# Kernel tuning notes

Measured on AMD Instinct MI355X. Metric: run time of the kernel, lower is better.

The kernel has to match this reference:

```python
import jax, jax.numpy as jnp
import numpy as np

N, D = 16384, 2048


def setup_inputs() -> dict:
    key = jax.random.key(0)
    k1, k2, k3, k4 = jax.random.split(key, 4)
    X = jax.random.normal(k1, (N, D), dtype=jnp.float32)
    keep = jax.random.uniform(k4, (N, D)) > 0.5
    X = jnp.where(keep, X, 0.0)
    A = jax.random.normal(k2, (D, D), dtype=jnp.float32)
    b = jax.random.normal(k3, (D,), dtype=jnp.float32)
    return {"X": X, "A": A, "b": b}


def reference(X, A, b):
    # y_pred = X @ A.T + b
    y_pred = jnp.einsum('nd,kd->nk', X, A) + b  # [N, D]
    mask = X != 0
    masked = jnp.where(mask, y_pred, 0.0)
    row_sum = masked.sum(axis=1, keepdims=True)          # [N, 1]
    has_any = mask.any(axis=1, keepdims=True)            # [N, 1]
    y_out = jnp.where(mask, masked / row_sum, 0.0)
    # rows with an empty mask stay all-zero (matches the Python-loop guard)
    y_out = jnp.where(has_any, y_out, 0.0)
    return y_out
```

## Files before the change

kernel.cpp:

```cpp
#include <hip/hip_runtime.h>

#define N_ROWS 16384
#define D_DIM  2048
#define BM 128
#define BN 128
#define BK 32
#define NKT (D_DIM / BK)

typedef __attribute__((ext_vector_type(8)))  _Float16 half8;
typedef __attribute__((ext_vector_type(4)))  _Float16 half4_t;
typedef __attribute__((ext_vector_type(4)))  float floatx4;

typedef __attribute__((address_space(1))) const unsigned int as1_uint;
typedef __attribute__((address_space(3))) unsigned int as3_uint;

__device__ __forceinline__ void gload_lds16(const _Float16* g, _Float16* l) {
    __builtin_amdgcn_global_load_lds((as1_uint*)g, (as3_uint*)l, 16, 0, 0);
}

__global__ void split_all_kernel(const float4* __restrict__ Xs,
                                 half4_t* __restrict__ Xdh,
                                 half4_t* __restrict__ Xdl,
                                 unsigned char* __restrict__ mask,
                                 const float4* __restrict__ As,
                                 half4_t* __restrict__ Adh,
                                 half4_t* __restrict__ Adl,
                                 int nX8, int total8)
{
    int i = blockIdx.x * blockDim.x + threadIdx.x;
    if (i >= total8) return;

    const float4* src; half4_t* dh; half4_t* dl; int j; bool domask;
    if (i < nX8) { src = Xs; dh = Xdh; dl = Xdl; j = i;       domask = true;  }
    else         { src = As; dh = Adh; dl = Adl; j = i - nX8; domask = false; }

    float4 a = src[2 * j];
    float4 b = src[2 * j + 1];
    half4_t ha, la, hb, lb;
    ha[0] = (_Float16)a.x; ha[1] = (_Float16)a.y;
    ha[2] = (_Float16)a.z; ha[3] = (_Float16)a.w;
    la[0] = (_Float16)((a.x - (float)ha[0]) * 4096.0f);
    la[1] = (_Float16)((a.y - (float)ha[1]) * 4096.0f);
    la[2] = (_Float16)((a.z - (float)ha[2]) * 4096.0f);
    la[3] = (_Float16)((a.w - (float)ha[3]) * 4096.0f);
    hb[0] = (_Float16)b.x; hb[1] = (_Float16)b.y;
    hb[2] = (_Float16)b.z; hb[3] = (_Float16)b.w;
    lb[0] = (_Float16)((b.x - (float)hb[0]) * 4096.0f);
    lb[1] = (_Float16)((b.y - (float)hb[1]) * 4096.0f);
    lb[2] = (_Float16)((b.z - (float)hb[2]) * 4096.0f);
    lb[3] = (_Float16)((b.w - (float)hb[3]) * 4096.0f);
    dh[2 * j] = ha; dh[2 * j + 1] = hb;
    dl[2 * j] = la; dl[2 * j + 1] = lb;
    if (domask) {
        unsigned int m = 0;
        m |= (a.x != 0.0f) ? 0x01u : 0u;  m |= (a.y != 0.0f) ? 0x02u : 0u;
        m |= (a.z != 0.0f) ? 0x04u : 0u;  m |= (a.w != 0.0f) ? 0x08u : 0u;
        m |= (b.x != 0.0f) ? 0x10u : 0u;  m |= (b.y != 0.0f) ? 0x20u : 0u;
        m |= (b.z != 0.0f) ? 0x40u : 0u;  m |= (b.w != 0.0f) ? 0x80u : 0u;
        mask[j] = (unsigned char)m;
    }
}

__global__ __launch_bounds__(256, 2)
void gemm_presplit_kernel(const _Float16* __restrict__ Xh,
                          const _Float16* __restrict__ Xl,
                          const _Float16* __restrict__ Ah,
                          const _Float16* __restrict__ Al,
                          const unsigned char* __restrict__ maskbits,
                          const float* __restrict__ bias,
                          float* __restrict__ out,
                          float* __restrict__ partials)
{
    __shared__ __align__(16) _Float16 sXh[2][BM * BK];
    __shared__ __align__(16) _Float16 sXl[2][BM * BK];
    __shared__ __align__(16) _Float16 sAh[2][BN * BK];
    __shared__ __align__(16) _Float16 sAl[2][BN * BK];

    const int t   = threadIdx.x;
    const int bid = blockIdx.x;

    const int xcd    = bid & 7;
    const int local  = bid >> 3;
    const int r_tile = (xcd << 4) + (local & 15);
    const int c_tile = local >> 4;
    const int m0 = r_tile * BM;
    const int n0 = c_tile * BN;

    const int lane  = t & 63;
    const int w     = t >> 6;
    const int wr    = w >> 1;
    const int wc    = w & 1;
    const int lrow  = lane & 15;
    const int lslot = lane >> 4;

    floatx4 acc1[4][4], acc2[4][4];
    #pragma unroll
    for (int mi = 0; mi < 4; ++mi)
        #pragma unroll
        for (int ni = 0; ni < 4; ++ni)
            #pragma unroll
            for (int j = 0; j < 4; ++j) { acc1[mi][ni][j] = 0.f; acc2[mi][ni][j] = 0.f; }

    const _Float16* gsrc;
    _Float16* lb0; _Float16* lb1;
    if      (w == 0) { gsrc = Xh + (size_t)m0 * D_DIM; lb0 = &sXh[0][0]; lb1 = &sXh[1][0]; }
    else if (w == 1) { gsrc = Xl + (size_t)m0 * D_DIM; lb0 = &sXl[0][0]; lb1 = &sXl[1][0]; }
    else if (w == 2) { gsrc = Ah + (size_t)n0 * D_DIM; lb0 = &sAh[0][0]; lb1 = &sAh[1][0]; }
    else             { gsrc = Al + (size_t)n0 * D_DIM; lb0 = &sAl[0][0]; lb1 = &sAl[1][0]; }

    int off8[8];
    #pragma unroll
    for (int i = 0; i < 8; ++i) {
        int c = i * 64 + lane;
        int row = c >> 2;
        int sp  = c & 3;
        int kslot = sp ^ ((row >> 1) & 3);
        off8[i] = row * D_DIM + kslot * 8;
    }

    auto issue = [&](int buf, int kt) {
        _Float16* lb = buf ? lb1 : lb0;
        const _Float16* gk = gsrc + kt * BK;
        #pragma unroll
        for (int i = 0; i < 8; ++i)
            gload_lds16(gk + off8[i], lb + i * 512);
    };

    issue(0, 0);

    int cur = 0;
    for (int kt = 0; kt < NKT; ++kt) {
        __syncthreads();
        if (kt + 1 < NKT) issue(cur ^ 1, kt + 1);

        half8 bhf[4], blf[4];
        #pragma unroll
        for (int ni = 0; ni < 4; ++ni) {
            int row = wc * 64 + ni * 16 + lrow;
            int off = row * BK + ((lslot ^ ((row >> 1) & 3)) << 3);
            bhf[ni] = *reinterpret_cast<const half8*>(&sAh[cur][off]);
            blf[ni] = *reinterpret_cast<const half8*>(&sAl[cur][off]);
        }
        #pragma unroll
        for (int mi = 0; mi < 4; ++mi) {
            int row = wr * 64 + mi * 16 + lrow;
            int off = row * BK + ((lslot ^ ((row >> 1) & 3)) << 3);
            half8 ah = *reinterpret_cast<const half8*>(&sXh[cur][off]);
            half8 al = *reinterpret_cast<const half8*>(&sXl[cur][off]);
            #pragma unroll
            for (int ni = 0; ni < 4; ++ni) {
                acc1[mi][ni] = __builtin_amdgcn_mfma_f32_16x16x32_f16(ah, bhf[ni], acc1[mi][ni], 0, 0, 0);
                acc2[mi][ni] = __builtin_amdgcn_mfma_f32_16x16x32_f16(ah, blf[ni], acc2[mi][ni], 0, 0, 0);
                acc2[mi][ni] = __builtin_amdgcn_mfma_f32_16x16x32_f16(al, bhf[ni], acc2[mi][ni], 0, 0, 0);
            }
        }
        cur ^= 1;
    }

    #pragma unroll
    for (int mi = 0; mi < 4; ++mi) {
        float rs[4];
        #pragma unroll
        for (int j = 0; j < 4; ++j) rs[j] = 0.f;
        #pragma unroll
        for (int ni = 0; ni < 4; ++ni) {
            int c = n0 + wc * 64 + ni * 16 + lrow;
            float bv = bias[c];
            #pragma unroll
            for (int j = 0; j < 4; ++j) {
                int r = m0 + wr * 64 + mi * 16 + lslot * 4 + j;
                size_t idx = (size_t)r * D_DIM + c;
                float v = acc1[mi][ni][j] + acc2[mi][ni][j] * (1.0f / 4096.0f) + bv;
                unsigned int bit = (maskbits[idx >> 3] >> (c & 7)) & 1u;
                float mv = bit ? v : 0.0f;
                out[idx] = mv;
                rs[j] += mv;
            }
        }
        #pragma unroll
        for (int j = 0; j < 4; ++j) {
            float s = rs[j];
            s += __shfl_xor(s, 1, 64);
            s += __shfl_xor(s, 2, 64);
            s += __shfl_xor(s, 4, 64);
            s += __shfl_xor(s, 8, 64);
            if (lrow == 0) {
                int r = m0 + wr * 64 + mi * 16 + lslot * 4 + j;
                partials[(size_t)r * 32 + c_tile * 2 + wc] = s;
            }
        }
    }
}

__global__ void scale_fused_kernel(float* __restrict__ out,
                                   const float* __restrict__ partials)
{
    int r   = blockIdx.x * 8 + (threadIdx.x >> 5);
    int l32 = threadIdx.x & 31;
    float s = partials[(size_t)r * 32 + l32];
    s += __shfl_xor(s, 1, 32);
    s += __shfl_xor(s, 2, 32);
    s += __shfl_xor(s, 4, 32);
    s += __shfl_xor(s, 8, 32);
    s += __shfl_xor(s, 16, 32);
    float inv = (s != 0.0f) ? (1.0f / s) : 0.0f;
    float4* rowp = reinterpret_cast<float4*>(out + (size_t)r * D_DIM);
    #pragma unroll
    for (int j = 0; j < 16; ++j) {
        float4 v = rowp[j * 32 + l32];
        v.x *= inv; v.y *= inv; v.z *= inv; v.w *= inv;
        rowp[j * 32 + l32] = v;
    }
}

__global__ __launch_bounds__(256, 2)
void gemm_mask_kernel(const float* __restrict__ X,
                      const float* __restrict__ A,
                      const float* __restrict__ bias,
                      float* __restrict__ out)
{
    __shared__ __align__(16) _Float16 sXh[2][BM * BK];
    __shared__ __align__(16) _Float16 sXl[2][BM * BK];
    __shared__ __align__(16) _Float16 sAh[2][BN * BK];
    __shared__ __align__(16) _Float16 sAl[2][BN * BK];

    const int t   = threadIdx.x;
    const int bid = blockIdx.x;
    const int xcd    = bid & 7;
    const int local  = bid >> 3;
    const int r_tile = (xcd << 4) + (local & 15);
    const int c_tile = local >> 4;
    const int m0 = r_tile * BM;
    const int n0 = c_tile * BN;

    const int lane  = t & 63;
    const int w     = t >> 6;
    const int wr    = w >> 1;
    const int wc    = w & 1;
    const int lrow  = lane & 15;
    const int lslot = lane >> 4;

    const float4* X4 = reinterpret_cast<const float4*>(X);
    const float4* A4 = reinterpret_cast<const float4*>(A);

    floatx4 acc1[4][4], acc2[4][4];
    #pragma unroll
    for (int mi = 0; mi < 4; ++mi)
        #pragma unroll
        for (int ni = 0; ni < 4; ++ni)
            #pragma unroll
            for (int j = 0; j < 4; ++j) { acc1[mi][ni][j] = 0.f; acc2[mi][ni][j] = 0.f; }

    float4 rx[4], ra[4];
    #pragma unroll
    for (int i = 0; i < 4; ++i) {
        int f = i * 256 + t; int row = f >> 3; int k4 = f & 7;
        rx[i] = X4[(size_t)(m0 + row) * (D_DIM / 4) + k4];
        ra[i] = A4[(size_t)(n0 + row) * (D_DIM / 4) + k4];
    }

    auto stage = [&](const float4* rv, _Float16* dsh, _Float16* dsl) {
        #pragma unroll
        for (int i = 0; i < 4; ++i) {
            int f = i * 256 + t; int row = f >> 3; int k4 = f & 7;
            float4 v = rv[i];
            half4_t h, l;
            h[0] = (_Float16)v.x; h[1] = (_Float16)v.y;
            h[2] = (_Float16)v.z; h[3] = (_Float16)v.w;
            l[0] = (_Float16)((v.x - (float)h[0]) * 4096.0f);
            l[1] = (_Float16)((v.y - (float)h[1]) * 4096.0f);
            l[2] = (_Float16)((v.z - (float)h[2]) * 4096.0f);
            l[3] = (_Float16)((v.w - (float)h[3]) * 4096.0f);
            int off = row * BK + ((((k4 >> 1) ^ ((row >> 1) & 3)) << 3) + ((k4 & 1) << 2));
            *reinterpret_cast<half4_t*>(dsh + off) = h;
            *reinterpret_cast<half4_t*>(dsl + off) = l;
        }
    };

    stage(rx, &sXh[0][0], &sXl[0][0]);
    stage(ra, &sAh[0][0], &sAl[0][0]);

    int cur = 0;
    for (int kt = 0; kt < NKT; ++kt) {
        __syncthreads();
        const bool more = (kt + 1 < NKT);
        if (more) {
            int kb = (kt + 1) * (BK / 4);
            #pragma unroll
            for (int i = 0; i < 4; ++i) {
                int f = i * 256 + t; int row = f >> 3; int k4 = f & 7;
                rx[i] = X4[(size_t)(m0 + row) * (D_DIM / 4) + kb + k4];
                ra[i] = A4[(size_t)(n0 + row) * (D_DIM / 4) + kb + k4];
            }
        }

        half8 bhf[4], blf[4];
        #pragma unroll
        for (int ni = 0; ni < 4; ++ni) {
            int row = wc * 64 + ni * 16 + lrow;
            int off = row * BK + ((lslot ^ ((row >> 1) & 3)) << 3);
            bhf[ni] = *reinterpret_cast<const half8*>(&sAh[cur][off]);
            blf[ni] = *reinterpret_cast<const half8*>(&sAl[cur][off]);
        }
        #pragma unroll
        for (int mi = 0; mi < 4; ++mi) {
            int row = wr * 64 + mi * 16 + lrow;
            int off = row * BK + ((lslot ^ ((row >> 1) & 3)) << 3);
            half8 ah = *reinterpret_cast<const half8*>(&sXh[cur][off]);
            half8 al = *reinterpret_cast<const half8*>(&sXl[cur][off]);
            #pragma unroll
            for (int ni = 0; ni < 4; ++ni) {
                acc1[mi][ni] = __builtin_amdgcn_mfma_f32_16x16x32_f16(ah, bhf[ni], acc1[mi][ni], 0, 0, 0);
                acc2[mi][ni] = __builtin_amdgcn_mfma_f32_16x16x32_f16(ah, blf[ni], acc2[mi][ni], 0, 0, 0);
                acc2[mi][ni] = __builtin_amdgcn_mfma_f32_16x16x32_f16(al, bhf[ni], acc2[mi][ni], 0, 0, 0);
            }
        }

        if (more) {
            int nxt = cur ^ 1;
            stage(rx, &sXh[nxt][0], &sXl[nxt][0]);
            stage(ra, &sAh[nxt][0], &sAl[nxt][0]);
            cur = nxt;
        }
    }

    #pragma unroll
    for (int mi = 0; mi < 4; ++mi) {
        #pragma unroll
        for (int ni = 0; ni < 4; ++ni) {
            int c = n0 + wc * 64 + ni * 16 + lrow;
            float bv = bias[c];
            #pragma unroll
            for (int j = 0; j < 4; ++j) {
                int r = m0 + wr * 64 + mi * 16 + lslot * 4 + j;
                float v = acc1[mi][ni][j] + acc2[mi][ni][j] * (1.0f / 4096.0f) + bv;
                float xv = X[(size_t)r * D_DIM + c];
                out[(size_t)r * D_DIM + c] = (xv != 0.0f) ? v : 0.0f;
            }
        }
    }
}

__global__ void row_sum_inv_kernel(const float* __restrict__ out, float* __restrict__ inv)
{
    int gw = (blockIdx.x * 256 + threadIdx.x) >> 6;
    int l  = threadIdx.x & 63;
    const float4* row = reinterpret_cast<const float4*>(out) + (size_t)gw * (D_DIM / 4);
    float s = 0.f;
    #pragma unroll
    for (int j = 0; j < 8; ++j) {
        float4 v = row[j * 64 + l];
        s += (v.x + v.y) + (v.z + v.w);
    }
    #pragma unroll
    for (int off = 32; off > 0; off >>= 1) s += __shfl_down(s, off, 64);
    if (l == 0) inv[gw] = (s != 0.0f) ? (1.0f / s) : 0.0f;
}

__global__ void scale_kernel(float* __restrict__ out, const float* __restrict__ inv)
{
    const int total = N_ROWS * (D_DIM / 4);
    float4* o = reinterpret_cast<float4*>(out);
    for (int i = blockIdx.x * blockDim.x + threadIdx.x; i < total;
         i += gridDim.x * blockDim.x) {
        float s  = inv[i >> 9];
        float4 v = o[i];
        v.x *= s; v.y *= s; v.z *= s; v.w *= s;
        o[i] = v;
    }
}

extern "C" void kernel_launch(void* const* d_in, const int* in_sizes, int n_in,
                              void* d_out, int out_size, void* d_ws, size_t ws_size,
                              hipStream_t stream)
{
    const float* X  = (const float*)d_in[0];
    const float* A  = (const float*)d_in[1];
    const float* b  = (const float*)d_in[2];
    float* out = (float*)d_out;

    const size_t nX = (size_t)N_ROWS * D_DIM;
    const size_t nA = (size_t)D_DIM * D_DIM;
    const size_t part_bytes = (size_t)N_ROWS * 32 * sizeof(float);
    const size_t mask_bytes = nX / 8;
    const size_t need = part_bytes + 2 * nX * 2 + 2 * nA * 2 + mask_bytes;

    if (ws_size >= need) {
        float*         part = (float*)d_ws;
        _Float16*      Xh   = (_Float16*)((char*)d_ws + part_bytes);
        _Float16*      Xl   = Xh + nX;
        _Float16*      Ah   = Xl + nX;
        _Float16*      Al   = Ah + nA;
        unsigned char* mb   = (unsigned char*)(Al + nA);

        const int nX8    = (int)(nX / 8);
        const int total8 = (int)((nX + nA) / 8);
        hipLaunchKernelGGL(split_all_kernel, dim3((total8 + 255) / 256), dim3(256), 0, stream,
                           (const float4*)X, (half4_t*)Xh, (half4_t*)Xl, mb,
                           (const float4*)A, (half4_t*)Ah, (half4_t*)Al,
                           nX8, total8);
        hipLaunchKernelGGL(gemm_presplit_kernel, dim3((N_ROWS / BM) * (D_DIM / BN)), dim3(256), 0, stream,
                           Xh, Xl, Ah, Al, mb, b, out, part);
        hipLaunchKernelGGL(scale_fused_kernel, dim3(N_ROWS / 8), dim3(256), 0, stream,
                           out, part);
    } else {
        float* inv = (float*)d_ws;
        hipLaunchKernelGGL(gemm_mask_kernel, dim3((N_ROWS / BM) * (D_DIM / BN)), dim3(256), 0, stream,
                           X, A, b, out);
        hipLaunchKernelGGL(row_sum_inv_kernel, dim3(N_ROWS / 4), dim3(256), 0, stream, out, inv);
        hipLaunchKernelGGL(scale_kernel, dim3(2048), dim3(256), 0, stream, out, inv);
    }
}
```

Measured before the change: 475.2 us.

## Use 8 waves per GEMM block with 2x4 warp layout

Doubles the GEMM workgroup from 256 to 512 threads. Each wave now covers a 64x32 output sub-tile instead of 64x64, and the async global-to-LDS loads are split across twice as many waves. Per-row partial sums widen from 32 to 64 per row, and the scale kernel is adjusted to reduce 64 partials per row with one wave. The intent is more waves per CU to hide latency and lower accumulator register pressure, at the cost of fewer MFMAs per LDS fragment load (less register-level reuse of the A fragments).

```diff
diff --git a/kernel.cpp b/kernel.cpp
--- a/kernel.cpp
+++ b/kernel.cpp
@@ -61,15 +61,15 @@
     }
 }
 
-__global__ __launch_bounds__(256, 2)
-void gemm_presplit_kernel(const _Float16* __restrict__ Xh,
-                          const _Float16* __restrict__ Xl,
-                          const _Float16* __restrict__ Ah,
-                          const _Float16* __restrict__ Al,
-                          const unsigned char* __restrict__ maskbits,
-                          const float* __restrict__ bias,
-                          float* __restrict__ out,
-                          float* __restrict__ partials)
+__global__ __launch_bounds__(512, 2)
+void gemm_presplit8_kernel(const _Float16* __restrict__ Xh,
+                           const _Float16* __restrict__ Xl,
+                           const _Float16* __restrict__ Ah,
+                           const _Float16* __restrict__ Al,
+                           const unsigned char* __restrict__ maskbits,
+                           const float* __restrict__ bias,
+                           float* __restrict__ out,
+                           float* __restrict__ partials)
 {
     __shared__ __align__(16) _Float16 sXh[2][BM * BK];
     __shared__ __align__(16) _Float16 sXl[2][BM * BK];
@@ -88,42 +88,44 @@
 
     const int lane  = t & 63;
     const int w     = t >> 6;
-    const int wr    = w >> 1;
-    const int wc    = w & 1;
+    const int wr    = w >> 2;
+    const int wc    = w & 3;
     const int lrow  = lane & 15;
     const int lslot = lane >> 4;
 
-    floatx4 acc1[4][4], acc2[4][4];
+    floatx4 acc1[4][2], acc2[4][2];
     #pragma unroll
     for (int mi = 0; mi < 4; ++mi)
         #pragma unroll
-        for (int ni = 0; ni < 4; ++ni)
+        for (int ni = 0; ni < 2; ++ni)
             #pragma unroll
             for (int j = 0; j < 4; ++j) { acc1[mi][ni][j] = 0.f; acc2[mi][ni][j] = 0.f; }
 
     const _Float16* gsrc;
     _Float16* lb0; _Float16* lb1;
-    if      (w == 0) { gsrc = Xh + (size_t)m0 * D_DIM; lb0 = &sXh[0][0]; lb1 = &sXh[1][0]; }
-    else if (w == 1) { gsrc = Xl + (size_t)m0 * D_DIM; lb0 = &sXl[0][0]; lb1 = &sXl[1][0]; }
-    else if (w == 2) { gsrc = Ah + (size_t)n0 * D_DIM; lb0 = &sAh[0][0]; lb1 = &sAh[1][0]; }
-    else             { gsrc = Al + (size_t)n0 * D_DIM; lb0 = &sAl[0][0]; lb1 = &sAl[1][0]; }
-
-    int off8[8];
-    #pragma unroll
-    for (int i = 0; i < 8; ++i) {
-        int c = i * 64 + lane;
+    const int arr = w & 3;
+    if      (arr == 0) { gsrc = Xh + (size_t)m0 * D_DIM; lb0 = &sXh[0][0]; lb1 = &sXh[1][0]; }
+    else if (arr == 1) { gsrc = Xl + (size_t)m0 * D_DIM; lb0 = &sXl[0][0]; lb1 = &sXl[1][0]; }
+    else if (arr == 2) { gsrc = Ah + (size_t)n0 * D_DIM; lb0 = &sAh[0][0]; lb1 = &sAh[1][0]; }
+    else               { gsrc = Al + (size_t)n0 * D_DIM; lb0 = &sAl[0][0]; lb1 = &sAl[1][0]; }
+    const int cbase = (w >> 2) * 256;
+
+    int off4[4];
+    #pragma unroll
+    for (int i = 0; i < 4; ++i) {
+        int c = cbase + i * 64 + lane;
         int row = c >> 2;
         int sp  = c & 3;
         int kslot = sp ^ ((row >> 1) & 3);
-        off8[i] = row * D_DIM + kslot * 8;
+        off4[i] = row * D_DIM + kslot * 8;
     }
 
     auto issue = [&](int buf, int kt) {
-        _Float16* lb = buf ? lb1 : lb0;
+        _Float16* lb = (buf ? lb1 : lb0) + cbase * 8;
         const _Float16* gk = gsrc + kt * BK;
         #pragma unroll
-        for (int i = 0; i < 8; ++i)
-            gload_lds16(gk + off8[i], lb + i * 512);
+        for (int i = 0; i < 4; ++i)
+            gload_lds16(gk + off4[i], lb + i * 512);
     };
 
     issue(0, 0);
@@ -133,10 +135,10 @@
         __syncthreads();
         if (kt + 1 < NKT) issue(cur ^ 1, kt + 1);
 
-        half8 bhf[4], blf[4];
-        #pragma unroll
-        for (int ni = 0; ni < 4; ++ni) {
-            int row = wc * 64 + ni * 16 + lrow;
+        half8 bhf[2], blf[2];
+        #pragma unroll
+        for (int ni = 0; ni < 2; ++ni) {
+            int row = wc * 32 + ni * 16 + lrow;
             int off = row * BK + ((lslot ^ ((row >> 1) & 3)) << 3);
             bhf[ni] = *reinterpret_cast<const half8*>(&sAh[cur][off]);
             blf[ni] = *reinterpret_cast<const half8*>(&sAl[cur][off]);
@@ -148,7 +150,7 @@
             half8 ah = *reinterpret_cast<const half8*>(&sXh[cur][off]);
             half8 al = *reinterpret_cast<const half8*>(&sXl[cur][off]);
             #pragma unroll
-            for (int ni = 0; ni < 4; ++ni) {
+            for (int ni = 0; ni < 2; ++ni) {
                 acc1[mi][ni] = __builtin_amdgcn_mfma_f32_16x16x32_f16(ah, bhf[ni], acc1[mi][ni], 0, 0, 0);
                 acc2[mi][ni] = __builtin_amdgcn_mfma_f32_16x16x32_f16(ah, blf[ni], acc2[mi][ni], 0, 0, 0);
                 acc2[mi][ni] = __builtin_amdgcn_mfma_f32_16x16x32_f16(al, bhf[ni], acc2[mi][ni], 0, 0, 0);
@@ -163,8 +165,8 @@
         #pragma unroll
         for (int j = 0; j < 4; ++j) rs[j] = 0.f;
         #pragma unroll
-        for (int ni = 0; ni < 4; ++ni) {
-            int c = n0 + wc * 64 + ni * 16 + lrow;
+        for (int ni = 0; ni < 2; ++ni) {
+            int c = n0 + wc * 32 + ni * 16 + lrow;
             float bv = bias[c];
             #pragma unroll
             for (int j = 0; j < 4; ++j) {
@@ -186,7 +188,7 @@
             s += __shfl_xor(s, 8, 64);
             if (lrow == 0) {
                 int r = m0 + wr * 64 + mi * 16 + lslot * 4 + j;
-                partials[(size_t)r * 32 + c_tile * 2 + wc] = s;
+                partials[(size_t)r * 64 + c_tile * 4 + wc] = s;
             }
         }
     }
@@ -195,21 +197,22 @@
 __global__ void scale_fused_kernel(float* __restrict__ out,
                                    const float* __restrict__ partials)
 {
-    int r   = blockIdx.x * 8 + (threadIdx.x >> 5);
-    int l32 = threadIdx.x & 31;
-    float s = partials[(size_t)r * 32 + l32];
-    s += __shfl_xor(s, 1, 32);
-    s += __shfl_xor(s, 2, 32);
-    s += __shfl_xor(s, 4, 32);
-    s += __shfl_xor(s, 8, 32);
-    s += __shfl_xor(s, 16, 32);
+    int r    = blockIdx.x * 4 + (threadIdx.x >> 6);
+    int lane = threadIdx.x & 63;
+    float s = partials[(size_t)r * 64 + lane];
+    s += __shfl_xor(s, 1, 64);
+    s += __shfl_xor(s, 2, 64);
+    s += __shfl_xor(s, 4, 64);
+    s += __shfl_xor(s, 8, 64);
+    s += __shfl_xor(s, 16, 64);
+    s += __shfl_xor(s, 32, 64);
     float inv = (s != 0.0f) ? (1.0f / s) : 0.0f;
     float4* rowp = reinterpret_cast<float4*>(out + (size_t)r * D_DIM);
     #pragma unroll
-    for (int j = 0; j < 16; ++j) {
-        float4 v = rowp[j * 32 + l32];
+    for (int j = 0; j < 8; ++j) {
+        float4 v = rowp[j * 64 + lane];
         v.x *= inv; v.y *= inv; v.z *= inv; v.w *= inv;
-        rowp[j * 32 + l32] = v;
+        rowp[j * 64 + lane] = v;
     }
 }
 
@@ -381,7 +384,7 @@
 
     const size_t nX = (size_t)N_ROWS * D_DIM;
     const size_t nA = (size_t)D_DIM * D_DIM;
-    const size_t part_bytes = (size_t)N_ROWS * 32 * sizeof(float);
+    const size_t part_bytes = (size_t)N_ROWS * 64 * sizeof(float);
     const size_t mask_bytes = nX / 8;
     const size_t need = part_bytes + 2 * nX * 2 + 2 * nA * 2 + mask_bytes;
 
@@ -399,9 +402,9 @@
                            (const float4*)X, (half4_t*)Xh, (half4_t*)Xl, mb,
                            (const float4*)A, (half4_t*)Ah, (half4_t*)Al,
                            nX8, total8);
-        hipLaunchKernelGGL(gemm_presplit_kernel, dim3((N_ROWS / BM) * (D_DIM / BN)), dim3(256), 0, stream,
+        hipLaunchKernelGGL(gemm_presplit8_kernel, dim3((N_ROWS / BM) * (D_DIM / BN)), dim3(512), 0, stream,
                            Xh, Xl, Ah, Al, mb, b, out, part);
-        hipLaunchKernelGGL(scale_fused_kernel, dim3(N_ROWS / 8), dim3(256), 0, stream,
+        hipLaunchKernelGGL(scale_fused_kernel, dim3(N_ROWS / 4), dim3(256), 0, stream,
                            out, part);
     } else {
         float* inv = (float*)d_ws;
```

After: 540.8 us. 1.14x slower.
